# Optimization experiments

Hardware: AMD Instinct MI355X
Metric: run time of the kernel (lower is better)

Reference implementation:

```python
import jax, jax.numpy as jnp
import numpy as np

B, N, F_IN, H, HID = 2, 1024, 128, 4, 32  # batch, nodes, in_feat, heads, hidden per head


def setup_inputs() -> dict:
    key = jax.random.key(0)
    k1, k2, k3, k4 = jax.random.split(key, 4)
    node_feat = jax.random.normal(k1, (B, N, F_IN), dtype=jnp.float32)
    adj_mtx = jax.random.randint(k2, (B, N, N), 0, 2, dtype=jnp.int32)  # 0/1 adjacency
    # xavier_normal init for params
    W = jax.random.normal(k3, (F_IN, H * HID), dtype=jnp.float32) * np.sqrt(2.0 / (F_IN + H * HID))
    Wa = jax.random.normal(k4, (H, HID), dtype=jnp.float32) * np.sqrt(2.0 / (H + HID))
    return {"node_feat": node_feat, "adj_mtx": adj_mtx, "W": W, "Wa": Wa}


def reference(node_feat, adj_mtx, W, Wa):
    b, n, _ = node_feat.shape
    h, hid = Wa.shape
    # projected features: (B, H, N, hid)
    x = (node_feat @ W).reshape(b, n, h, hid).transpose(0, 2, 1, 3)
    # GATv2 additive scores: leaky_relu(x_i + x_j) . Wa  -> (B, H, N, N)
    s = jax.nn.leaky_relu(x[:, :, :, None, :] + x[:, :, None, :, :], negative_slope=0.2)
    e = jnp.einsum('bhijk,hk->bhij', s, Wa)
    # mask non-edges, softmax over neighbors j
    e = jnp.where(adj_mtx[:, None, :, :] > 0, e, -jnp.inf)
    att = jax.nn.softmax(e, axis=-1)
    # aggregate values: (B, H, N, hid)
    xp = jnp.einsum('bhij,bhjd->bhid', att, x)
    # concat heads -> (B, N, H*hid)
    return xp.transpose(0, 2, 1, 3).reshape(b, n, h * hid)
```

## Files before the change

kernel.cpp:

```cpp
#include <hip/hip_runtime.h>
#include <math.h>

#define BB 2
#define NN 1024
#define HH 4
#define F_IN 128
#define HID 32
#define TJ 64
#define NT 16
#define NC 2
#define CT (NT/NC)

#define LOG2E 1.44269504f

typedef unsigned long long u64;
typedef unsigned int u32;
typedef _Float16 f16;
typedef _Float16 h2   __attribute__((ext_vector_type(2)));
typedef _Float16 f16x4 __attribute__((ext_vector_type(4)));
typedef _Float16 f16x8 __attribute__((ext_vector_type(8)));
typedef float f32x4 __attribute__((ext_vector_type(4)));

#define WS_XH  0
#define WS_D6  524288
#define WS_XT  557056
#define WS_P   1081344
#define WS_LS  17858560

#if __has_builtin(__builtin_amdgcn_fdot2)
#define FDOT2(a, b, c) __builtin_amdgcn_fdot2((a), (b), (c), false)
#else
static __device__ __forceinline__ float FDOT2(h2 a, h2 b, float c) {
    return fmaf((float)a[0], (float)b[0], fmaf((float)a[1], (float)b[1], c));
}
#endif

template <typename D, typename S>
static __device__ __forceinline__ D bcast(S s) { return __builtin_bit_cast(D, s); }

__global__ __launch_bounds__(128) void gat_proj_kernel(const float* __restrict__ feat,
        const float* __restrict__ W, const float* __restrict__ Wa,
        f16* __restrict__ xh, f16* __restrict__ xt, float* __restrict__ d6) {
    const int RPB = 4;
    int blk = blockIdx.x;
    int b  = blk / (NN / RPB);
    int n0 = (blk % (NN / RPB)) * RPB;
    int t  = threadIdx.x;

    __shared__ float fs[RPB][F_IN];
#pragma unroll
    for (int e = 0; e < RPB; ++e) {
        int idx = e * 128 + t;
        int r = idx >> 7, f = idx & 127;
        fs[r][f] = feat[((size_t)(b*NN + n0 + r))*F_IN + f];
    }
    __syncthreads();

    float acc[RPB];
#pragma unroll
    for (int r = 0; r < RPB; ++r) acc[r] = 0.f;
    for (int f = 0; f < F_IN; ++f) {
        float w = W[f*(HH*HID) + t];
#pragma unroll
        for (int r = 0; r < RPB; ++r) acc[r] = fmaf(fs[r][f], w, acc[r]);
    }

    int h = t >> 5, k = t & 31;
    int bh = b*HH + h;
#pragma unroll
    for (int r = 0; r < RPB; ++r)
        xh[((size_t)bh*NN + n0 + r)*HID + k] = (f16)acc[r];
    {
        f16x4 hv;
#pragma unroll
        for (int r = 0; r < RPB; ++r) hv[r] = (f16)acc[r];
        *(f16x4*)(xt + ((size_t)bh*HID + k)*NN + n0) = hv;
    }
    float w_t = Wa[t];
#pragma unroll
    for (int r = 0; r < RPB; ++r) {
        float p = acc[r] * w_t;
#pragma unroll
        for (int off = 16; off >= 1; off >>= 1) p += __shfl_xor(p, off, 32);
        if (k == 0) d6[(size_t)bh*NN + n0 + r] = 0.6f * LOG2E * p;
    }
}

__device__ __forceinline__ u32 srfl(u32 v) { return __builtin_amdgcn_readfirstlane(v); }

__global__ __launch_bounds__(256) void gat_score_kernel(const f16* __restrict__ xh,
                                                        const float* __restrict__ d6,
                                                        const int* __restrict__ adj,
                                                        const float* __restrict__ Wa,
                                                        f16* __restrict__ P,
                                                        float* __restrict__ lsp) {
    const int tid = threadIdx.x;
    const int w = __builtin_amdgcn_readfirstlane(tid >> 6);
    const int l = tid & 63;
    const int blk = blockIdx.x;
    const int bh = blk & 7;
    const int rest = blk >> 3;
    const int jc = rest & (NC - 1);
    const int i0 = (rest >> 1) << 4;
    const int h = bh & 3, b = bh >> 2;
    const int ib = i0 + 4*w;

    const u32* xhu = (const u32*)(xh + (size_t)bh*NN*HID);
    const float* dbh = d6 + (size_t)bh*NN;

    u32 wa2[16];
    {
        const float* wap = Wa + h*HID;
#pragma unroll
        for (int q = 0; q < 16; ++q) {
            h2 hw;
            hw[0] = (f16)((0.4f*LOG2E) * wap[2*q]);
            hw[1] = (f16)((0.4f*LOG2E) * wap[2*q+1]);
            wa2[q] = srfl(bcast<u32>(hw));
        }
    }
    u32 xi2[4][16];
    float ci[4];
#pragma unroll
    for (int r = 0; r < 4; ++r) {
        const u32* xr = xhu + (size_t)(ib + r)*16;
#pragma unroll
        for (int q = 0; q < 16; ++q) xi2[r][q] = srfl(xr[q]);
        ci[r] = __uint_as_float(srfl(__float_as_uint(dbh[ib + r]))) - 8.0f;
    }

    const int* adj0 = adj + ((size_t)b*NN + ib + 0)*NN;
    const int* adj1 = adj + ((size_t)b*NN + ib + 1)*NN;
    const int* adj2 = adj + ((size_t)b*NN + ib + 2)*NN;
    const int* adj3 = adj + ((size_t)b*NN + ib + 3)*NN;
    f16* pr0 = P + ((size_t)bh << 20) + (size_t)(ib + 0)*NN;
    f16* pr1 = P + ((size_t)bh << 20) + (size_t)(ib + 1)*NN;
    f16* pr2 = P + ((size_t)bh << 20) + (size_t)(ib + 2)*NN;
    f16* pr3 = P + ((size_t)bh << 20) + (size_t)(ib + 3)*NN;

    float ls0 = 0.f, ls1 = 0.f, ls2 = 0.f, ls3 = 0.f;

    for (int tt = 0; tt < CT; ++tt) {
        const int j = (jc*CT + tt)*TJ + l;
        u64 m0 = __ballot(adj0[j] > 0);
        u64 m1 = __ballot(adj1[j] > 0);
        u64 m2 = __ballot(adj2[j] > 0);
        u64 m3 = __ballot(adj3[j] > 0);
        float dj = dbh[j];

        const u32* xjp = xhu + (size_t)j*16;
        uint4 xa = *(const uint4*)(xjp);
        uint4 xb = *(const uint4*)(xjp + 4);
        uint4 xc = *(const uint4*)(xjp + 8);
        uint4 xd = *(const uint4*)(xjp + 12);
        u32 xj[16] = {xa.x, xa.y, xa.z, xa.w, xb.x, xb.y, xb.z, xb.w,
                      xc.x, xc.y, xc.z, xc.w, xd.x, xd.y, xd.z, xd.w};

        float s0 = 0.f, s1 = 0.f, s2 = 0.f, s3 = 0.f;
#pragma unroll
        for (int q = 0; q < 16; ++q) {
            h2 xjh = bcast<h2>(xj[q]);
            h2 wq  = bcast<h2>(wa2[q]);
            h2 v; u32 a;
            v = bcast<h2>(xi2[0][q]) + xjh; a = bcast<u32>(v) & 0x7fff7fffu;
            s0 = FDOT2(bcast<h2>(a), wq, s0);
            v = bcast<h2>(xi2[1][q]) + xjh; a = bcast<u32>(v) & 0x7fff7fffu;
            s1 = FDOT2(bcast<h2>(a), wq, s1);
            v = bcast<h2>(xi2[2][q]) + xjh; a = bcast<u32>(v) & 0x7fff7fffu;
            s2 = FDOT2(bcast<h2>(a), wq, s2);
            v = bcast<h2>(xi2[3][q]) + xjh; a = bcast<u32>(v) & 0x7fff7fffu;
            s3 = FDOT2(bcast<h2>(a), wq, s3);
        }
        float p0 = exp2f(ci[0] + dj + s0);
        float p1 = exp2f(ci[1] + dj + s1);
        float p2 = exp2f(ci[2] + dj + s2);
        float p3 = exp2f(ci[3] + dj + s3);
        asm("v_cndmask_b32 %0, 0, %1, %2" : "=v"(p0) : "v"(p0), "s"(m0));
        asm("v_cndmask_b32 %0, 0, %1, %2" : "=v"(p1) : "v"(p1), "s"(m1));
        asm("v_cndmask_b32 %0, 0, %1, %2" : "=v"(p2) : "v"(p2), "s"(m2));
        asm("v_cndmask_b32 %0, 0, %1, %2" : "=v"(p3) : "v"(p3), "s"(m3));
        ls0 += p0; ls1 += p1; ls2 += p2; ls3 += p3;
        pr0[j] = (f16)p0;
        pr1[j] = (f16)p1;
        pr2[j] = (f16)p2;
        pr3[j] = (f16)p3;
    }

#pragma unroll
    for (int off = 32; off >= 1; off >>= 1) {
        ls0 += __shfl_xor(ls0, off, 64);
        ls1 += __shfl_xor(ls1, off, 64);
        ls2 += __shfl_xor(ls2, off, 64);
        ls3 += __shfl_xor(ls3, off, 64);
    }
    if (l == 0) {
        float* lp = lsp + (size_t)jc*(8*NN) + bh*NN + ib;
        lp[0] = ls0; lp[1] = ls1; lp[2] = ls2; lp[3] = ls3;
    }
}

__global__ __launch_bounds__(64) void gat_agg_kernel(const f16* __restrict__ P,
                                                     const f16* __restrict__ xt,
                                                     const float* __restrict__ lsp,
                                                     float* __restrict__ out) {
    const int l = threadIdx.x;
    const int blk = blockIdx.x;
    const int bh = blk & 7;
    const int it = blk >> 3;
    const int i0 = it << 4;
    const int b = bh >> 2, h = bh & 3;

    const f16* Pb  = P  + ((size_t)bh << 20);
    const f16* xtb = xt + (size_t)bh * HID * NN;

    f32x4 acc0 = {0.f, 0.f, 0.f, 0.f};
    f32x4 acc1 = {0.f, 0.f, 0.f, 0.f};
    const int lrow = l & 15, lslot = (l >> 4) << 3;

#pragma unroll
    for (int jt = 0; jt < 32; ++jt) {
        const int joff = jt*32 + lslot;
        f16x8 af = *(const f16x8*)(Pb  + (size_t)(i0 + lrow)*NN + joff);
        f16x8 b0 = *(const f16x8*)(xtb + (size_t)lrow*NN + joff);
        f16x8 b1 = *(const f16x8*)(xtb + (size_t)(16 + lrow)*NN + joff);
        acc0 = __builtin_amdgcn_mfma_f32_16x16x32_f16(af, b0, acc0, 0, 0, 0);
        acc1 = __builtin_amdgcn_mfma_f32_16x16x32_f16(af, b1, acc1, 0, 0, 0);
    }

#pragma unroll
    for (int r = 0; r < 4; ++r) {
        int row = i0 + ((l >> 4) << 2) + r;
        float ls = lsp[bh*NN + row] + lsp[8*NN + bh*NN + row];
        float inv = 1.0f / ls;
        float* orow = out + ((size_t)(b*NN + row))*(HH*HID) + h*HID;
        orow[lrow]      = acc0[r] * inv;
        orow[16 + lrow] = acc1[r] * inv;
    }
}

extern "C" void kernel_launch(void* const* d_in, const int* in_sizes, int n_in,
                              void* d_out, int out_size, void* d_ws, size_t ws_size,
                              hipStream_t stream) {
    const float* node_feat = (const float*)d_in[0];
    const int*   adj_mtx   = (const int*)d_in[1];
    const float* W         = (const float*)d_in[2];
    const float* Wa        = (const float*)d_in[3];
    float* out = (float*)d_out;

    char* ws = (char*)d_ws;
    f16*   xh_ws = (f16*)(ws + WS_XH);
    float* d6_ws = (float*)(ws + WS_D6);
    f16*   xt_ws = (f16*)(ws + WS_XT);
    f16*   P_ws  = (f16*)(ws + WS_P);
    float* ls_ws = (float*)(ws + WS_LS);

    hipLaunchKernelGGL(gat_proj_kernel, dim3(BB*NN/4), dim3(128), 0, stream,
                       node_feat, W, Wa, xh_ws, xt_ws, d6_ws);
    hipLaunchKernelGGL(gat_score_kernel, dim3(8 * (NN/16) * NC), dim3(256), 0, stream,
                       xh_ws, d6_ws, adj_mtx, Wa, P_ws, ls_ws);
    hipLaunchKernelGGL(gat_agg_kernel, dim3(8 * (NN/16)), dim3(64), 0, stream,
                       P_ws, xt_ws, ls_ws, out);
}
```

Measured before the change: 39.81 us.

## Fuse attention score and aggregation kernels, keeping probabilities in shared memory

Merges the score kernel and the aggregation kernel into one 512-thread block per 16 query rows. Unnormalized probabilities now stay in LDS instead of a 16 MB fp16 global buffer. Each wave computes two rows over all j and then runs an MFMA on its own j-slice, and the partial sums are reduced across waves through shared memory. This removes the global P round-trip and one launch. In exchange each block needs more LDS, there are fewer blocks in the grid, and a cross-wave reduction step is added.

```diff
diff --git a/kernel.cpp b/kernel.cpp
--- a/kernel.cpp
+++ b/kernel.cpp
@@ -8,15 +8,13 @@
 #define HID 32
 #define TJ 64
 #define NT 16
-#define NC 2
-#define CT (NT/NC)
 
 #define LOG2E 1.44269504f
 
 typedef unsigned long long u64;
 typedef unsigned int u32;
 typedef _Float16 f16;
-typedef _Float16 h2   __attribute__((ext_vector_type(2)));
+typedef _Float16 h2    __attribute__((ext_vector_type(2)));
 typedef _Float16 f16x4 __attribute__((ext_vector_type(4)));
 typedef _Float16 f16x8 __attribute__((ext_vector_type(8)));
 typedef float f32x4 __attribute__((ext_vector_type(4)));
@@ -24,8 +22,6 @@
 #define WS_XH  0
 #define WS_D6  524288
 #define WS_XT  557056
-#define WS_P   1081344
-#define WS_LS  17858560
 
 #if __has_builtin(__builtin_amdgcn_fdot2)
 #define FDOT2(a, b, c) __builtin_amdgcn_fdot2((a), (b), (c), false)
@@ -88,25 +84,28 @@
 
 __device__ __forceinline__ u32 srfl(u32 v) { return __builtin_amdgcn_readfirstlane(v); }
 
-__global__ __launch_bounds__(256) void gat_score_kernel(const f16* __restrict__ xh,
+__global__ __launch_bounds__(512) void gat_fused_kernel(const f16* __restrict__ xh,
                                                         const float* __restrict__ d6,
                                                         const int* __restrict__ adj,
                                                         const float* __restrict__ Wa,
-                                                        f16* __restrict__ P,
-                                                        float* __restrict__ lsp) {
+                                                        const f16* __restrict__ xt,
+                                                        float* __restrict__ out) {
     const int tid = threadIdx.x;
     const int w = __builtin_amdgcn_readfirstlane(tid >> 6);
     const int l = tid & 63;
     const int blk = blockIdx.x;
     const int bh = blk & 7;
-    const int rest = blk >> 3;
-    const int jc = rest & (NC - 1);
-    const int i0 = (rest >> 1) << 4;
+    const int i0 = (blk >> 3) << 4;
     const int h = bh & 3, b = bh >> 2;
-    const int ib = i0 + 4*w;
+    const int rA = 2*w, rB = 2*w + 1;
+    const int iA = i0 + rA, iB = i0 + rB;
 
     const u32* xhu = (const u32*)(xh + (size_t)bh*NN*HID);
     const float* dbh = d6 + (size_t)bh*NN;
+
+    __shared__ __align__(16) f16 Pl[16][1032];
+    __shared__ float scr[8][64][9];
+    __shared__ float lsinv[16];
 
     u32 wa2[16];
     {
@@ -119,33 +118,25 @@
             wa2[q] = srfl(bcast<u32>(hw));
         }
     }
-    u32 xi2[4][16];
-    float ci[4];
-#pragma unroll
-    for (int r = 0; r < 4; ++r) {
-        const u32* xr = xhu + (size_t)(ib + r)*16;
-#pragma unroll
-        for (int q = 0; q < 16; ++q) xi2[r][q] = srfl(xr[q]);
-        ci[r] = __uint_as_float(srfl(__float_as_uint(dbh[ib + r]))) - 8.0f;
-    }
-
-    const int* adj0 = adj + ((size_t)b*NN + ib + 0)*NN;
-    const int* adj1 = adj + ((size_t)b*NN + ib + 1)*NN;
-    const int* adj2 = adj + ((size_t)b*NN + ib + 2)*NN;
-    const int* adj3 = adj + ((size_t)b*NN + ib + 3)*NN;
-    f16* pr0 = P + ((size_t)bh << 20) + (size_t)(ib + 0)*NN;
-    f16* pr1 = P + ((size_t)bh << 20) + (size_t)(ib + 1)*NN;
-    f16* pr2 = P + ((size_t)bh << 20) + (size_t)(ib + 2)*NN;
-    f16* pr3 = P + ((size_t)bh << 20) + (size_t)(ib + 3)*NN;
-
-    float ls0 = 0.f, ls1 = 0.f, ls2 = 0.f, ls3 = 0.f;
-
-    for (int tt = 0; tt < CT; ++tt) {
-        const int j = (jc*CT + tt)*TJ + l;
-        u64 m0 = __ballot(adj0[j] > 0);
-        u64 m1 = __ballot(adj1[j] > 0);
-        u64 m2 = __ballot(adj2[j] > 0);
-        u64 m3 = __ballot(adj3[j] > 0);
+    u32 xiA[16], xiB[16];
+    {
+        const u32* xrA = xhu + (size_t)iA*16;
+        const u32* xrB = xhu + (size_t)iB*16;
+#pragma unroll
+        for (int q = 0; q < 16; ++q) { xiA[q] = srfl(xrA[q]); xiB[q] = srfl(xrB[q]); }
+    }
+    float ciA = __uint_as_float(srfl(__float_as_uint(dbh[iA]))) - 8.0f;
+    float ciB = __uint_as_float(srfl(__float_as_uint(dbh[iB]))) - 8.0f;
+
+    const int* adjA = adj + ((size_t)b*NN + iA)*NN;
+    const int* adjB = adj + ((size_t)b*NN + iB)*NN;
+
+    float lsA = 0.f, lsB = 0.f;
+
+    for (int tt = 0; tt < NT; ++tt) {
+        const int j = tt*TJ + l;
+        u64 mA = __ballot(adjA[j] > 0);
+        u64 mB = __ballot(adjB[j] > 0);
         float dj = dbh[j];
 
         const u32* xjp = xhu + (size_t)j*16;
@@ -156,71 +147,44 @@
         u32 xj[16] = {xa.x, xa.y, xa.z, xa.w, xb.x, xb.y, xb.z, xb.w,
                       xc.x, xc.y, xc.z, xc.w, xd.x, xd.y, xd.z, xd.w};
 
-        float s0 = 0.f, s1 = 0.f, s2 = 0.f, s3 = 0.f;
+        float sA = 0.f, sB = 0.f;
 #pragma unroll
         for (int q = 0; q < 16; ++q) {
             h2 xjh = bcast<h2>(xj[q]);
             h2 wq  = bcast<h2>(wa2[q]);
             h2 v; u32 a;
-            v = bcast<h2>(xi2[0][q]) + xjh; a = bcast<u32>(v) & 0x7fff7fffu;
-            s0 = FDOT2(bcast<h2>(a), wq, s0);
-            v = bcast<h2>(xi2[1][q]) + xjh; a = bcast<u32>(v) & 0x7fff7fffu;
-            s1 = FDOT2(bcast<h2>(a), wq, s1);
-            v = bcast<h2>(xi2[2][q]) + xjh; a = bcast<u32>(v) & 0x7fff7fffu;
-            s2 = FDOT2(bcast<h2>(a), wq, s2);
-            v = bcast<h2>(xi2[3][q]) + xjh; a = bcast<u32>(v) & 0x7fff7fffu;
-            s3 = FDOT2(bcast<h2>(a), wq, s3);
+            v = bcast<h2>(xiA[q]) + xjh; a = bcast<u32>(v) & 0x7fff7fffu;
+            sA = FDOT2(bcast<h2>(a), wq, sA);
+            v = bcast<h2>(xiB[q]) + xjh; a = bcast<u32>(v) & 0x7fff7fffu;
+            sB = FDOT2(bcast<h2>(a), wq, sB);
         }
-        float p0 = exp2f(ci[0] + dj + s0);
-        float p1 = exp2f(ci[1] + dj + s1);
-        float p2 = exp2f(ci[2] + dj + s2);
-        float p3 = exp2f(ci[3] + dj + s3);
-        asm("v_cndmask_b32 %0, 0, %1, %2" : "=v"(p0) : "v"(p0), "s"(m0));
-        asm("v_cndmask_b32 %0, 0, %1, %2" : "=v"(p1) : "v"(p1), "s"(m1));
-        asm("v_cndmask_b32 %0, 0, %1, %2" : "=v"(p2) : "v"(p2), "s"(m2));
-        asm("v_cndmask_b32 %0, 0, %1, %2" : "=v"(p3) : "v"(p3), "s"(m3));
-        ls0 += p0; ls1 += p1; ls2 += p2; ls3 += p3;
-        pr0[j] = (f16)p0;
-        pr1[j] = (f16)p1;
-        pr2[j] = (f16)p2;
-        pr3[j] = (f16)p3;
+        float pA = exp2f(ciA + dj + sA);
+        float pB = exp2f(ciB + dj + sB);
+        asm("v_cndmask_b32 %0, 0, %1, %2" : "=v"(pA) : "v"(pA), "s"(mA));
+        asm("v_cndmask_b32 %0, 0, %1, %2" : "=v"(pB) : "v"(pB), "s"(mB));
+        lsA += pA;
+        lsB += pB;
+        Pl[rA][j] = (f16)pA;
+        Pl[rB][j] = (f16)pB;
     }
 
 #pragma unroll
     for (int off = 32; off >= 1; off >>= 1) {
-        ls0 += __shfl_xor(ls0, off, 64);
-        ls1 += __shfl_xor(ls1, off, 64);
-        ls2 += __shfl_xor(ls2, off, 64);
-        ls3 += __shfl_xor(ls3, off, 64);
-    }
-    if (l == 0) {
-        float* lp = lsp + (size_t)jc*(8*NN) + bh*NN + ib;
-        lp[0] = ls0; lp[1] = ls1; lp[2] = ls2; lp[3] = ls3;
-    }
-}
-
-__global__ __launch_bounds__(64) void gat_agg_kernel(const f16* __restrict__ P,
-                                                     const f16* __restrict__ xt,
-                                                     const float* __restrict__ lsp,
-                                                     float* __restrict__ out) {
-    const int l = threadIdx.x;
-    const int blk = blockIdx.x;
-    const int bh = blk & 7;
-    const int it = blk >> 3;
-    const int i0 = it << 4;
-    const int b = bh >> 2, h = bh & 3;
-
-    const f16* Pb  = P  + ((size_t)bh << 20);
+        lsA += __shfl_xor(lsA, off, 64);
+        lsB += __shfl_xor(lsB, off, 64);
+    }
+    if (l == 0) { lsinv[rA] = 1.0f / lsA; lsinv[rB] = 1.0f / lsB; }
+    __syncthreads();
+
     const f16* xtb = xt + (size_t)bh * HID * NN;
+    const int lrow = l & 15, lslot = (l >> 4) << 3;
 
     f32x4 acc0 = {0.f, 0.f, 0.f, 0.f};
     f32x4 acc1 = {0.f, 0.f, 0.f, 0.f};
-    const int lrow = l & 15, lslot = (l >> 4) << 3;
-
-#pragma unroll
-    for (int jt = 0; jt < 32; ++jt) {
-        const int joff = jt*32 + lslot;
-        f16x8 af = *(const f16x8*)(Pb  + (size_t)(i0 + lrow)*NN + joff);
+#pragma unroll
+    for (int q = 0; q < 4; ++q) {
+        const int joff = (w*4 + q)*32 + lslot;
+        f16x8 af = *(const f16x8*)&Pl[lrow][joff];
         f16x8 b0 = *(const f16x8*)(xtb + (size_t)lrow*NN + joff);
         f16x8 b1 = *(const f16x8*)(xtb + (size_t)(16 + lrow)*NN + joff);
         acc0 = __builtin_amdgcn_mfma_f32_16x16x32_f16(af, b0, acc0, 0, 0, 0);
@@ -228,13 +192,21 @@
     }
 
 #pragma unroll
-    for (int r = 0; r < 4; ++r) {
-        int row = i0 + ((l >> 4) << 2) + r;
-        float ls = lsp[bh*NN + row] + lsp[8*NN + bh*NN + row];
-        float inv = 1.0f / ls;
-        float* orow = out + ((size_t)(b*NN + row))*(HH*HID) + h*HID;
-        orow[lrow]      = acc0[r] * inv;
-        orow[16 + lrow] = acc1[r] * inv;
+    for (int e = 0; e < 4; ++e) {
+        scr[w][l][e]     = acc0[e];
+        scr[w][l][4 + e] = acc1[e];
+    }
+    __syncthreads();
+
+    {
+        float s = 0.f;
+#pragma unroll
+        for (int ww = 0; ww < 8; ++ww) s += scr[ww][l][w];
+        const int r = w & 3;
+        const int col = ((w >= 4) ? 16 : 0) + lrow;
+        const int rloc = ((l >> 4) << 2) + r;
+        const int row = i0 + rloc;
+        out[((size_t)(b*NN + row))*(HH*HID) + h*HID + col] = s * lsinv[rloc];
     }
 }
 
@@ -251,13 +223,9 @@
     f16*   xh_ws = (f16*)(ws + WS_XH);
     float* d6_ws = (float*)(ws + WS_D6);
     f16*   xt_ws = (f16*)(ws + WS_XT);
-    f16*   P_ws  = (f16*)(ws + WS_P);
-    float* ls_ws = (float*)(ws + WS_LS);
 
     hipLaunchKernelGGL(gat_proj_kernel, dim3(BB*NN/4), dim3(128), 0, stream,
                        node_feat, W, Wa, xh_ws, xt_ws, d6_ws);
-    hipLaunchKernelGGL(gat_score_kernel, dim3(8 * (NN/16) * NC), dim3(256), 0, stream,
-                       xh_ws, d6_ws, adj_mtx, Wa, P_ws, ls_ws);
-    hipLaunchKernelGGL(gat_agg_kernel, dim3(8 * (NN/16)), dim3(64), 0, stream,
-                       P_ws, xt_ws, ls_ws, out);
-}
+    hipLaunchKernelGGL(gat_fused_kernel, dim3(8 * (NN/16)), dim3(512), 0, stream,
+                       xh_ws, d6_ws, adj_mtx, Wa, xt_ws, out);
+}
```

After: 37.21 us. -6.5%, faster.

## Fuse score and aggregation kernels, keeping attention probabilities in LDS

Applied to the files above, without the earlier changes.

Merges the score and aggregation kernels into one 512-thread block per 16 rows and head. The unnormalized probabilities stay in shared memory instead of a 16 MB global P buffer, and the row sums are reduced in LDS. Each wave computes a partial MFMA over its own j-slice, and the partials are summed through a shared scratch array. This removes the global write and reread of P and one kernel launch. In exchange it adds about 66 KB of LDS per block and two block-wide barriers, which may reduce occupancy.

```diff
diff --git a/kernel.cpp b/kernel.cpp
--- a/kernel.cpp
+++ b/kernel.cpp
@@ -8,15 +8,14 @@
 #define HID 32
 #define TJ 64
 #define NT 16
-#define NC 2
-#define CT (NT/NC)
+#define CT 8
 
 #define LOG2E 1.44269504f
 
 typedef unsigned long long u64;
 typedef unsigned int u32;
 typedef _Float16 f16;
-typedef _Float16 h2   __attribute__((ext_vector_type(2)));
+typedef _Float16 h2    __attribute__((ext_vector_type(2)));
 typedef _Float16 f16x4 __attribute__((ext_vector_type(4)));
 typedef _Float16 f16x8 __attribute__((ext_vector_type(8)));
 typedef float f32x4 __attribute__((ext_vector_type(4)));
@@ -24,8 +23,6 @@
 #define WS_XH  0
 #define WS_D6  524288
 #define WS_XT  557056
-#define WS_P   1081344
-#define WS_LS  17858560
 
 #if __has_builtin(__builtin_amdgcn_fdot2)
 #define FDOT2(a, b, c) __builtin_amdgcn_fdot2((a), (b), (c), false)
@@ -88,25 +85,28 @@
 
 __device__ __forceinline__ u32 srfl(u32 v) { return __builtin_amdgcn_readfirstlane(v); }
 
-__global__ __launch_bounds__(256) void gat_score_kernel(const f16* __restrict__ xh,
+__global__ __launch_bounds__(512) void gat_fused_kernel(const f16* __restrict__ xh,
                                                         const float* __restrict__ d6,
                                                         const int* __restrict__ adj,
                                                         const float* __restrict__ Wa,
-                                                        f16* __restrict__ P,
-                                                        float* __restrict__ lsp) {
+                                                        const f16* __restrict__ xt,
+                                                        float* __restrict__ out) {
     const int tid = threadIdx.x;
     const int w = __builtin_amdgcn_readfirstlane(tid >> 6);
     const int l = tid & 63;
     const int blk = blockIdx.x;
     const int bh = blk & 7;
-    const int rest = blk >> 3;
-    const int jc = rest & (NC - 1);
-    const int i0 = (rest >> 1) << 4;
+    const int i0 = (blk >> 3) << 4;
     const int h = bh & 3, b = bh >> 2;
-    const int ib = i0 + 4*w;
+    const int q4 = w & 3, hf = w >> 2;
+    const int ib = i0 + 4*q4;
 
     const u32* xhu = (const u32*)(xh + (size_t)bh*NN*HID);
     const float* dbh = d6 + (size_t)bh*NN;
+
+    __shared__ __align__(16) f16 Pl[16][1032];
+    __shared__ float scr[8][64][9];
+    __shared__ float lsp2[2][16];
 
     u32 wa2[16];
     {
@@ -133,15 +133,11 @@
     const int* adj1 = adj + ((size_t)b*NN + ib + 1)*NN;
     const int* adj2 = adj + ((size_t)b*NN + ib + 2)*NN;
     const int* adj3 = adj + ((size_t)b*NN + ib + 3)*NN;
-    f16* pr0 = P + ((size_t)bh << 20) + (size_t)(ib + 0)*NN;
-    f16* pr1 = P + ((size_t)bh << 20) + (size_t)(ib + 1)*NN;
-    f16* pr2 = P + ((size_t)bh << 20) + (size_t)(ib + 2)*NN;
-    f16* pr3 = P + ((size_t)bh << 20) + (size_t)(ib + 3)*NN;
 
     float ls0 = 0.f, ls1 = 0.f, ls2 = 0.f, ls3 = 0.f;
 
     for (int tt = 0; tt < CT; ++tt) {
-        const int j = (jc*CT + tt)*TJ + l;
+        const int j = (hf*CT + tt)*TJ + l;
         u64 m0 = __ballot(adj0[j] > 0);
         u64 m1 = __ballot(adj1[j] > 0);
         u64 m2 = __ballot(adj2[j] > 0);
@@ -180,10 +176,10 @@
         asm("v_cndmask_b32 %0, 0, %1, %2" : "=v"(p2) : "v"(p2), "s"(m2));
         asm("v_cndmask_b32 %0, 0, %1, %2" : "=v"(p3) : "v"(p3), "s"(m3));
         ls0 += p0; ls1 += p1; ls2 += p2; ls3 += p3;
-        pr0[j] = (f16)p0;
-        pr1[j] = (f16)p1;
-        pr2[j] = (f16)p2;
-        pr3[j] = (f16)p3;
+        Pl[4*q4 + 0][j] = (f16)p0;
+        Pl[4*q4 + 1][j] = (f16)p1;
+        Pl[4*q4 + 2][j] = (f16)p2;
+        Pl[4*q4 + 3][j] = (f16)p3;
     }
 
 #pragma unroll
@@ -194,33 +190,22 @@
         ls3 += __shfl_xor(ls3, off, 64);
     }
     if (l == 0) {
-        float* lp = lsp + (size_t)jc*(8*NN) + bh*NN + ib;
-        lp[0] = ls0; lp[1] = ls1; lp[2] = ls2; lp[3] = ls3;
-    }
-}
-
-__global__ __launch_bounds__(64) void gat_agg_kernel(const f16* __restrict__ P,
-                                                     const f16* __restrict__ xt,
-                                                     const float* __restrict__ lsp,
-                                                     float* __restrict__ out) {
-    const int l = threadIdx.x;
-    const int blk = blockIdx.x;
-    const int bh = blk & 7;
-    const int it = blk >> 3;
-    const int i0 = it << 4;
-    const int b = bh >> 2, h = bh & 3;
-
-    const f16* Pb  = P  + ((size_t)bh << 20);
+        lsp2[hf][4*q4 + 0] = ls0;
+        lsp2[hf][4*q4 + 1] = ls1;
+        lsp2[hf][4*q4 + 2] = ls2;
+        lsp2[hf][4*q4 + 3] = ls3;
+    }
+    __syncthreads();
+
     const f16* xtb = xt + (size_t)bh * HID * NN;
+    const int lrow = l & 15, lslot = (l >> 4) << 3;
 
     f32x4 acc0 = {0.f, 0.f, 0.f, 0.f};
     f32x4 acc1 = {0.f, 0.f, 0.f, 0.f};
-    const int lrow = l & 15, lslot = (l >> 4) << 3;
-
-#pragma unroll
-    for (int jt = 0; jt < 32; ++jt) {
-        const int joff = jt*32 + lslot;
-        f16x8 af = *(const f16x8*)(Pb  + (size_t)(i0 + lrow)*NN + joff);
+#pragma unroll
+    for (int q = 0; q < 4; ++q) {
+        const int joff = (w*4 + q)*32 + lslot;
+        f16x8 af = *(const f16x8*)&Pl[lrow][joff];
         f16x8 b0 = *(const f16x8*)(xtb + (size_t)lrow*NN + joff);
         f16x8 b1 = *(const f16x8*)(xtb + (size_t)(16 + lrow)*NN + joff);
         acc0 = __builtin_amdgcn_mfma_f32_16x16x32_f16(af, b0, acc0, 0, 0, 0);
@@ -228,13 +213,22 @@
     }
 
 #pragma unroll
-    for (int r = 0; r < 4; ++r) {
-        int row = i0 + ((l >> 4) << 2) + r;
-        float ls = lsp[bh*NN + row] + lsp[8*NN + bh*NN + row];
-        float inv = 1.0f / ls;
-        float* orow = out + ((size_t)(b*NN + row))*(HH*HID) + h*HID;
-        orow[lrow]      = acc0[r] * inv;
-        orow[16 + lrow] = acc1[r] * inv;
+    for (int e = 0; e < 4; ++e) {
+        scr[w][l][e]     = acc0[e];
+        scr[w][l][4 + e] = acc1[e];
+    }
+    __syncthreads();
+
+    {
+        float s = 0.f;
+#pragma unroll
+        for (int ww = 0; ww < 8; ++ww) s += scr[ww][l][w];
+        const int r = w & 3;
+        const int col = ((w >= 4) ? 16 : 0) + lrow;
+        const int rloc = ((l >> 4) << 2) + r;
+        const int row = i0 + rloc;
+        float inv = 1.0f / (lsp2[0][rloc] + lsp2[1][rloc]);
+        out[((size_t)(b*NN + row))*(HH*HID) + h*HID + col] = s * inv;
     }
 }
 
@@ -251,13 +245,9 @@
     f16*   xh_ws = (f16*)(ws + WS_XH);
     float* d6_ws = (float*)(ws + WS_D6);
     f16*   xt_ws = (f16*)(ws + WS_XT);
-    f16*   P_ws  = (f16*)(ws + WS_P);
-    float* ls_ws = (float*)(ws + WS_LS);
 
     hipLaunchKernelGGL(gat_proj_kernel, dim3(BB*NN/4), dim3(128), 0, stream,
                        node_feat, W, Wa, xh_ws, xt_ws, d6_ws);
-    hipLaunchKernelGGL(gat_score_kernel, dim3(8 * (NN/16) * NC), dim3(256), 0, stream,
-                       xh_ws, d6_ws, adj_mtx, Wa, P_ws, ls_ws);
-    hipLaunchKernelGGL(gat_agg_kernel, dim3(8 * (NN/16)), dim3(64), 0, stream,
-                       P_ws, xt_ws, ls_ws, out);
-}
+    hipLaunchKernelGGL(gat_fused_kernel, dim3(8 * (NN/16)), dim3(512), 0, stream,
+                       xh_ws, d6_ws, adj_mtx, Wa, xt_ws, out);
+}
```

Measured after the change: 35.79 us (median of 2 runs). 10.1% less time.
